# Kernel tuning notes

Hardware: AMD Instinct MI355X
Metric: run time of the kernel (lower is better)

Reference implementation:

```python
import jax, jax.numpy as jnp
import numpy as np

B, N, NODE_DIM, HID, HEAD = 32, 1024, 14, 64, 128
EDGE_PROB = 0.01


def setup_inputs() -> dict:
    key = jax.random.key(0)
    ks = jax.random.split(key, 12)
    x = jax.random.normal(ks[0], (B, N, NODE_DIM), dtype=jnp.float32)
    # sparse binary adjacency with self-loops (matches eye + edge scatter)
    adj = (jax.random.uniform(ks[1], (B, N, N)) < EDGE_PROB).astype(jnp.float32)
    adjacency = jnp.maximum(adj, jnp.eye(N, dtype=jnp.float32)[None])
    def lin(k, din, dout):
        kw, kb = jax.random.split(k)
        w = jax.random.normal(kw, (din, dout), dtype=jnp.float32) / np.sqrt(din)
        b = jnp.zeros((dout,), dtype=jnp.float32)
        return w, b
    W1, b1 = lin(ks[2], NODE_DIM, HID)
    W2, b2 = lin(ks[3], HID, HID)
    W3, b3 = lin(ks[4], HID, HID)
    Wf1, bf1 = lin(ks[5], HID, HEAD)
    Wf2, bf2 = lin(ks[6], HEAD, 1)
    return {"x": x, "adjacency": adjacency, "W1": W1, "b1": b1, "W2": W2,
            "b2": b2, "W3": W3, "b3": b3, "Wf1": Wf1, "bf1": bf1,
            "Wf2": Wf2, "bf2": bf2}


def _dense_graph_conv(x, norm_adj, W, b):
    # (D^-1/2 A D^-1/2) @ x, then linear
    return jnp.einsum('bnm,bmd->bnd', norm_adj, x) @ W + b


def reference(x, adjacency, W1, b1, W2, b2, W3, b3, Wf1, bf1, Wf2, bf2):
    degree = adjacency.sum(axis=-1)                      # [B,N]
    d_inv_sqrt = jnp.clip(degree, 1.0, None) ** -0.5
    norm_adj = d_inv_sqrt[..., :, None] * adjacency * d_inv_sqrt[..., None, :]
    h = jax.nn.relu(_dense_graph_conv(x, norm_adj, W1, b1))
    h = jax.nn.relu(_dense_graph_conv(h, norm_adj, W2, b2))
    h = jax.nn.relu(_dense_graph_conv(h, norm_adj, W3, b3))
    pooled = h.mean(axis=1)                              # [B,HID]
    return jax.nn.relu(pooled @ Wf1 + bf1) @ Wf2 + bf2   # [B,1]
```

## Files before the change

### kernel.cpp

```cpp
#include <hip/hip_runtime.h>
#include <math.h>

#define NN 1024
#define HID 64
#define HEADD 128
#define NODE_DIM 14
#define BATCH 32
#define CAP 64
#define ROWS (BATCH * NN)
#define ZROW ROWS
#define GROW (ROWS + 16)
#define RPW 8

__device__ __forceinline__ int swz4(int blk, int wv) {
    int x = blk & 7, q = blk >> 3;
    int batch = x + 8 * (q >> 8);
    return batch * NN + ((q & 255) << 2) + wv;
}
__device__ __forceinline__ int swz32(int blk, int wv) {
    int x = blk & 7, q = blk >> 3;
    int batch = x + 8 * (q >> 5);
    return batch * NN + ((q & 31) << 5) + wv * RPW;
}

__device__ __forceinline__ float rl_f(float v, int k) {
    return __int_as_float(__builtin_amdgcn_readlane(__float_as_int(v), k));
}
__device__ __forceinline__ float rfl_f(float v) {
    return __int_as_float(__builtin_amdgcn_readfirstlane(__float_as_int(v)));
}

__global__ __launch_bounds__(256) void k_build(const float* __restrict__ adj,
                                               const float* __restrict__ x,
                                               const float* __restrict__ W1,
                                               unsigned short* __restrict__ csr,
                                               int* __restrict__ nnz_g,
                                               float* __restrict__ dinv,
                                               float* __restrict__ g1,
                                               float* __restrict__ g2,
                                               float* __restrict__ g3,
                                               float* __restrict__ pooled) {
    __shared__ float sW1[NODE_DIM * HID];
    for (int i = threadIdx.x; i < NODE_DIM * HID; i += 256) sW1[i] = W1[i];
    if (blockIdx.x < 8) pooled[blockIdx.x * 256 + threadIdx.x] = 0.f;
    if (blockIdx.x == 8 && threadIdx.x < 64) {
        int t = threadIdx.x;
        g1[(size_t)ZROW * HID + t] = 0.f;
        g2[(size_t)ZROW * HID + t] = 0.f;
        g3[(size_t)ZROW * HID + t] = 0.f;
    }
    int wv = threadIdx.x >> 6, lane = threadIdx.x & 63;
    int row = swz4(blockIdx.x, wv);
    int brow = row & ~(NN - 1);
    const float4* rp = reinterpret_cast<const float4*>(adj + (size_t)row * NN);
    unsigned long long lt = ((unsigned long long)1 << lane) - 1;
    int base = 0;
#pragma unroll
    for (int j = 0; j < 4; ++j) {
        float4 v = rp[lane + 64 * j];
        float vv[4] = {v.x, v.y, v.z, v.w};
#pragma unroll
        for (int k = 0; k < 4; ++k) {
            unsigned long long mk = __ballot(vv[k] != 0.0f);
            if (mk) {
                if (vv[k] != 0.0f) {
                    int pos = base + __popcll(mk & lt);
                    if (pos < CAP)
                        csr[row * CAP + pos] =
                            (unsigned short)(brow + (lane + 64 * j) * 4 + k);
                }
                base += __popcll(mk);
            }
        }
    }
    float di = 1.0f / sqrtf((float)(base < 1 ? 1 : base));
    if (lane == 0) {
        nnz_g[row] = base < CAP ? base : CAP;
        dinv[row] = di;
    }
    __syncthreads();
    float acc = 0.f;
    const float* xr = x + (size_t)row * NODE_DIM;
#pragma unroll
    for (int d = 0; d < NODE_DIM; ++d) acc += xr[d] * sW1[d * HID + lane];
    g1[(size_t)row * HID + lane] = acc * di;
}

__device__ __forceinline__ void spmm8(const float* __restrict__ g_in,
                                      const int n[RPW], const int idx[RPW],
                                      int lane, float acc[RPW]) {
    int nmax = 1;
#pragma unroll
    for (int r = 0; r < RPW; ++r) { acc[r] = 0.f; nmax = n[r] > nmax ? n[r] : nmax; }
    float v[RPW];
#pragma unroll
    for (int r = 0; r < RPW; ++r) {
        int j = __builtin_amdgcn_readlane(idx[r], 0);
        v[r] = g_in[(size_t)j * HID + lane];
    }
    for (int k = 1; k < nmax; ++k) {
        float vn[RPW];
#pragma unroll
        for (int r = 0; r < RPW; ++r) {
            int j = __builtin_amdgcn_readlane(idx[r], k);
            vn[r] = g_in[(size_t)j * HID + lane];
        }
#pragma unroll
        for (int r = 0; r < RPW; ++r) { acc[r] += v[r]; v[r] = vn[r]; }
    }
#pragma unroll
    for (int r = 0; r < RPW; ++r) acc[r] += v[r];
}

__global__ __launch_bounds__(256, 6) void k_layer(const float* __restrict__ g_in,
                                                  const unsigned short* __restrict__ csr,
                                                  const int* __restrict__ nnz_g,
                                                  const float* __restrict__ dinv,
                                                  const float* __restrict__ bias,
                                                  const float* __restrict__ W,
                                                  float* __restrict__ g_out) {
    __shared__ float sW[HID * HID];
    {
        const float4* Wv = reinterpret_cast<const float4*>(W);
        float4* sWv = reinterpret_cast<float4*>(sW);
        for (int i = threadIdx.x; i < HID * HID / 4; i += 256) sWv[i] = Wv[i];
    }
    int wv = threadIdx.x >> 6, lane = threadIdx.x & 63;
    int row0 = swz32(blockIdx.x, wv);
    float bb = bias[lane];
    int n[RPW], idx[RPW];
    float dr[RPW];
#pragma unroll
    for (int r = 0; r < RPW; ++r) {
        int row = row0 + r;
        n[r] = __builtin_amdgcn_readfirstlane(nnz_g[row]);
        idx[r] = (lane < n[r]) ? (int)csr[row * CAP + lane] : ZROW;
        dr[r] = rfl_f(dinv[row]);
    }
    float acc[RPW];
    spmm8(g_in, n, idx, lane, acc);
    float h[RPW];
#pragma unroll
    for (int r = 0; r < RPW; ++r)
        h[r] = fmaxf(dr[r] * acc[r] + bb, 0.f) * dr[r];
    __syncthreads();
    float o[RPW];
#pragma unroll
    for (int r = 0; r < RPW; ++r) o[r] = 0.f;
#pragma unroll
    for (int d = 0; d < HID; ++d) {
        float w = sW[d * HID + lane];
#pragma unroll
        for (int r = 0; r < RPW; ++r) o[r] += rl_f(h[r], d) * w;
    }
#pragma unroll
    for (int r = 0; r < RPW; ++r)
        g_out[(size_t)(row0 + r) * HID + lane] = o[r];
}

__global__ __launch_bounds__(256, 6) void k_layer3(const float* __restrict__ g_in,
                                                   const unsigned short* __restrict__ csr,
                                                   const int* __restrict__ nnz_g,
                                                   const float* __restrict__ dinv,
                                                   const float* __restrict__ bias,
                                                   float* __restrict__ pooled) {
    __shared__ float sred[4][HID];
    int wv = threadIdx.x >> 6, lane = threadIdx.x & 63;
    int row0 = swz32(blockIdx.x, wv);
    float bb = bias[lane];
    int n[RPW], idx[RPW];
    float dr[RPW];
#pragma unroll
    for (int r = 0; r < RPW; ++r) {
        int row = row0 + r;
        n[r] = __builtin_amdgcn_readfirstlane(nnz_g[row]);
        idx[r] = (lane < n[r]) ? (int)csr[row * CAP + lane] : ZROW;
        dr[r] = rfl_f(dinv[row]);
    }
    float acc[RPW];
    spmm8(g_in, n, idx, lane, acc);
    float s = 0.f;
#pragma unroll
    for (int r = 0; r < RPW; ++r)
        s += fmaxf(dr[r] * acc[r] + bb, 0.f);
    sred[wv][lane] = s;
    __syncthreads();
    if (wv == 0) {
        float tot = sred[0][lane] + sred[1][lane] + sred[2][lane] + sred[3][lane];
        atomicAdd(&pooled[(row0 >> 10) * HID + lane], tot);
    }
}

__global__ __launch_bounds__(128) void k_head(const float* __restrict__ pooled_sum,
                                              const float* __restrict__ Wf1,
                                              const float* __restrict__ bf1,
                                              const float* __restrict__ Wf2,
                                              const float* __restrict__ bf2,
                                              float* __restrict__ out) {
    int b = blockIdx.x, t = threadIdx.x;
    __shared__ float p[HID];
    __shared__ float hid[HEADD];
    if (t < HID) p[t] = pooled_sum[b * HID + t] * (1.0f / NN);
    __syncthreads();
    float acc = bf1[t];
    for (int d = 0; d < HID; ++d) acc += p[d] * Wf1[d * HEADD + t];
    hid[t] = fmaxf(acc, 0.f);
    __syncthreads();
    if (t < 64) {
        float v = hid[t] * Wf2[t] + hid[t + 64] * Wf2[t + 64];
#pragma unroll
        for (int off = 32; off > 0; off >>= 1) v += __shfl_down(v, off, 64);
        if (t == 0) out[b] = v + bf2[0];
    }
}

extern "C" void kernel_launch(void* const* d_in, const int* in_sizes, int n_in,
                              void* d_out, int out_size, void* d_ws, size_t ws_size,
                              hipStream_t stream) {
    const float* x   = (const float*)d_in[0];
    const float* adj = (const float*)d_in[1];
    const float* W1  = (const float*)d_in[2];
    const float* b1  = (const float*)d_in[3];
    const float* W2  = (const float*)d_in[4];
    const float* b2  = (const float*)d_in[5];
    const float* W3  = (const float*)d_in[6];
    const float* b3  = (const float*)d_in[7];
    const float* Wf1 = (const float*)d_in[8];
    const float* bf1 = (const float*)d_in[9];
    const float* Wf2 = (const float*)d_in[10];
    const float* bf2 = (const float*)d_in[11];
    float* out = (float*)d_out;

    char* ws = (char*)d_ws;
    size_t off = 0;
    unsigned short* csr = (unsigned short*)(ws + off); off += (size_t)ROWS * CAP * 2;
    int*   nnz_g  = (int*)(ws + off);   off += (size_t)ROWS * 4;
    float* dinv   = (float*)(ws + off); off += (size_t)ROWS * 4;
    float* pooled = (float*)(ws + off); off += 4096 * 4;
    float* g1     = (float*)(ws + off); off += (size_t)GROW * HID * 4;
    float* g2     = (float*)(ws + off); off += (size_t)GROW * HID * 4;
    float* g3     = (float*)(ws + off);

    k_build <<<ROWS / 4, 256, 0, stream>>>(adj, x, W1, csr, nnz_g, dinv, g1, g2, g3, pooled);
    k_layer <<<ROWS / 32, 256, 0, stream>>>(g1, csr, nnz_g, dinv, b1, W2, g2);
    k_layer <<<ROWS / 32, 256, 0, stream>>>(g2, csr, nnz_g, dinv, b2, W3, g3);
    k_layer3<<<ROWS / 32, 256, 0, stream>>>(g3, csr, nnz_g, dinv, b3, pooled);
    k_head  <<<BATCH, 128, 0, stream>>>(pooled, Wf1, bf1, Wf2, bf2, out);
}
```

Measured before the change: 277.6 us.

## Fuse head MLP into last layer via last-block counter; unroll SpMM gather by two

The separate head kernel is removed. The final layer kernel now increments a global completion counter, and the last block to finish reads the pooled sums atomically and computes the MLP head for all batches. The SpMM gather loop is also unrolled by two, so that more independent loads are in flight per iteration. This saves one kernel launch at the cost of a serialized tail that runs on a single block, plus an extra atomic and fence in every block.

```diff
diff --git a/kernel.cpp b/kernel.cpp
--- a/kernel.cpp
+++ b/kernel.cpp
@@ -11,6 +11,7 @@
 #define ZROW ROWS
 #define GROW (ROWS + 16)
 #define RPW 8
+#define L3GRID (ROWS / 32)
 
 __device__ __forceinline__ int swz4(int blk, int wv) {
     int x = blk & 7, q = blk >> 3;
@@ -39,15 +40,19 @@
                                                float* __restrict__ g1,
                                                float* __restrict__ g2,
                                                float* __restrict__ g3,
-                                               float* __restrict__ pooled) {
+                                               float* __restrict__ pooled,
+                                               int* __restrict__ done) {
     __shared__ float sW1[NODE_DIM * HID];
     for (int i = threadIdx.x; i < NODE_DIM * HID; i += 256) sW1[i] = W1[i];
     if (blockIdx.x < 8) pooled[blockIdx.x * 256 + threadIdx.x] = 0.f;
-    if (blockIdx.x == 8 && threadIdx.x < 64) {
-        int t = threadIdx.x;
-        g1[(size_t)ZROW * HID + t] = 0.f;
-        g2[(size_t)ZROW * HID + t] = 0.f;
-        g3[(size_t)ZROW * HID + t] = 0.f;
+    if (blockIdx.x == 8) {
+        if (threadIdx.x < 64) {
+            int t = threadIdx.x;
+            g1[(size_t)ZROW * HID + t] = 0.f;
+            g2[(size_t)ZROW * HID + t] = 0.f;
+            g3[(size_t)ZROW * HID + t] = 0.f;
+        }
+        if (threadIdx.x == 64) *done = 0;
     }
     int wv = threadIdx.x >> 6, lane = threadIdx.x & 63;
     int row = swz4(blockIdx.x, wv);
@@ -92,24 +97,37 @@
     int nmax = 1;
 #pragma unroll
     for (int r = 0; r < RPW; ++r) { acc[r] = 0.f; nmax = n[r] > nmax ? n[r] : nmax; }
-    float v[RPW];
+    int m = (nmax + 1) & ~1;
+    float va[RPW], vb[RPW];
 #pragma unroll
     for (int r = 0; r < RPW; ++r) {
         int j = __builtin_amdgcn_readlane(idx[r], 0);
-        v[r] = g_in[(size_t)j * HID + lane];
-    }
-    for (int k = 1; k < nmax; ++k) {
-        float vn[RPW];
+        va[r] = g_in[(size_t)j * HID + lane];
+    }
+#pragma unroll
+    for (int r = 0; r < RPW; ++r) {
+        int j = __builtin_amdgcn_readlane(idx[r], 1);
+        vb[r] = g_in[(size_t)j * HID + lane];
+    }
+    for (int k = 2; k < m; k += 2) {
+        float na[RPW], nb[RPW];
 #pragma unroll
         for (int r = 0; r < RPW; ++r) {
             int j = __builtin_amdgcn_readlane(idx[r], k);
-            vn[r] = g_in[(size_t)j * HID + lane];
-        }
-#pragma unroll
-        for (int r = 0; r < RPW; ++r) { acc[r] += v[r]; v[r] = vn[r]; }
-    }
-#pragma unroll
-    for (int r = 0; r < RPW; ++r) acc[r] += v[r];
+            na[r] = g_in[(size_t)j * HID + lane];
+        }
+#pragma unroll
+        for (int r = 0; r < RPW; ++r) {
+            int j = __builtin_amdgcn_readlane(idx[r], k + 1);
+            nb[r] = g_in[(size_t)j * HID + lane];
+        }
+#pragma unroll
+        for (int r = 0; r < RPW; ++r) { acc[r] += va[r]; va[r] = na[r]; }
+#pragma unroll
+        for (int r = 0; r < RPW; ++r) { acc[r] += vb[r]; vb[r] = nb[r]; }
+    }
+#pragma unroll
+    for (int r = 0; r < RPW; ++r) acc[r] += va[r] + vb[r];
 }
 
 __global__ __launch_bounds__(256, 6) void k_layer(const float* __restrict__ g_in,
@@ -163,8 +181,15 @@
                                                    const int* __restrict__ nnz_g,
                                                    const float* __restrict__ dinv,
                                                    const float* __restrict__ bias,
-                                                   float* __restrict__ pooled) {
+                                                   float* __restrict__ pooled,
+                                                   const float* __restrict__ Wf1,
+                                                   const float* __restrict__ bf1,
+                                                   const float* __restrict__ Wf2,
+                                                   const float* __restrict__ bf2,
+                                                   float* __restrict__ out,
+                                                   int* __restrict__ done) {
     __shared__ float sred[4][HID];
+    __shared__ int s_last;
     int wv = threadIdx.x >> 6, lane = threadIdx.x & 63;
     int row0 = swz32(blockIdx.x, wv);
     float bb = bias[lane];
@@ -189,28 +214,36 @@
         float tot = sred[0][lane] + sred[1][lane] + sred[2][lane] + sred[3][lane];
         atomicAdd(&pooled[(row0 >> 10) * HID + lane], tot);
     }
-}
-
-__global__ __launch_bounds__(128) void k_head(const float* __restrict__ pooled_sum,
-                                              const float* __restrict__ Wf1,
-                                              const float* __restrict__ bf1,
-                                              const float* __restrict__ Wf2,
-                                              const float* __restrict__ bf2,
-                                              float* __restrict__ out) {
-    int b = blockIdx.x, t = threadIdx.x;
-    __shared__ float p[HID];
-    __shared__ float hid[HEADD];
-    if (t < HID) p[t] = pooled_sum[b * HID + t] * (1.0f / NN);
-    __syncthreads();
-    float acc = bf1[t];
-    for (int d = 0; d < HID; ++d) acc += p[d] * Wf1[d * HEADD + t];
-    hid[t] = fmaxf(acc, 0.f);
-    __syncthreads();
-    if (t < 64) {
-        float v = hid[t] * Wf2[t] + hid[t + 64] * Wf2[t + 64];
+    if (threadIdx.x == 0) {
+        __threadfence();
+        int c = atomicAdd(done, 1);
+        s_last = (c == L3GRID - 1);
+    }
+    __syncthreads();
+    if (!s_last) return;
+    __threadfence();
+
+    __shared__ float sp[2][HID];
+    __shared__ float spart[4];
+    int sub = threadIdx.x >> 7;
+    int t = threadIdx.x & 127;
+    float wb1 = bf1[t];
+    for (int it = 0; it < BATCH / 2; ++it) {
+        int b = it * 2 + sub;
+        if (t < HID)
+            sp[sub][t] = atomicAdd(&pooled[b * HID + t], 0.0f) * (1.0f / NN);
+        __syncthreads();
+        float acc2 = wb1;
+#pragma unroll 8
+        for (int d = 0; d < HID; ++d) acc2 += sp[sub][d] * Wf1[d * HEADD + t];
+        float v = fmaxf(acc2, 0.f) * Wf2[t];
 #pragma unroll
         for (int off = 32; off > 0; off >>= 1) v += __shfl_down(v, off, 64);
-        if (t == 0) out[b] = v + bf2[0];
+        if ((threadIdx.x & 63) == 0) spart[threadIdx.x >> 6] = v;
+        __syncthreads();
+        if (t == 0)
+            out[b] = spart[sub * 2] + spart[sub * 2 + 1] + bf2[0];
+        __syncthreads();
     }
 }
 
@@ -236,14 +269,15 @@
     unsigned short* csr = (unsigned short*)(ws + off); off += (size_t)ROWS * CAP * 2;
     int*   nnz_g  = (int*)(ws + off);   off += (size_t)ROWS * 4;
     float* dinv   = (float*)(ws + off); off += (size_t)ROWS * 4;
-    float* pooled = (float*)(ws + off); off += 4096 * 4;
+    float* pooled = (float*)(ws + off); off += 2048 * 4;
+    int*   done   = (int*)(ws + off);   off += 256;
     float* g1     = (float*)(ws + off); off += (size_t)GROW * HID * 4;
     float* g2     = (float*)(ws + off); off += (size_t)GROW * HID * 4;
     float* g3     = (float*)(ws + off);
 
-    k_build <<<ROWS / 4, 256, 0, stream>>>(adj, x, W1, csr, nnz_g, dinv, g1, g2, g3, pooled);
+    k_build <<<ROWS / 4, 256, 0, stream>>>(adj, x, W1, csr, nnz_g, dinv, g1, g2, g3, pooled, done);
     k_layer <<<ROWS / 32, 256, 0, stream>>>(g1, csr, nnz_g, dinv, b1, W2, g2);
     k_layer <<<ROWS / 32, 256, 0, stream>>>(g2, csr, nnz_g, dinv, b2, W3, g3);
-    k_layer3<<<ROWS / 32, 256, 0, stream>>>(g3, csr, nnz_g, dinv, b3, pooled);
-    k_head  <<<BATCH, 128, 0, stream>>>(pooled, Wf1, bf1, Wf2, bf2, out);
-}
+    k_layer3<<<L3GRID, 256, 0, stream>>>(g3, csr, nnz_g, dinv, b3, pooled,
+                                         Wf1, bf1, Wf2, bf2, out, done);
+}
```

Result: slower. 318.7 us (+14.8%).
